# Kernel tuning notes

Measured on AMD Instinct MI355X. Metric: run time of the kernel, lower is better.

The kernel has to match this reference:

```python
import jax, jax.numpy as jnp
import numpy as np

B, H, S, D = 2, 16, 2048, 128


def alibi_slopes(n_heads: int) -> jnp.ndarray:
    # Standard ALiBi geometric slopes: 2^(-8*(h+1)/n_heads)
    h = jnp.arange(n_heads, dtype=jnp.float32)
    return jnp.exp2(-8.0 * (h + 1.0) / n_heads)


def setup_inputs() -> dict:
    key = jax.random.key(0)
    kq, kk, kv = jax.random.split(key, 3)
    q = jax.random.normal(kq, (B, H, S, D), dtype=jnp.float32)
    k = jax.random.normal(kk, (B, H, S, D), dtype=jnp.float32)
    v = jax.random.normal(kv, (B, H, S, D), dtype=jnp.float32)
    return {"q": q, "k": k, "v": v}


def reference(q, k, v):
    # FlexAttention forward: causal block mask + ALiBi score_mod, default scale 1/sqrt(D)
    d = q.shape[-1]
    scale = 1.0 / jnp.sqrt(jnp.asarray(d, dtype=q.dtype))
    slopes = alibi_slopes(q.shape[1]).astype(q.dtype)  # [H]

    scores = jnp.einsum("bhqd,bhkd->bhqk", q, k) * scale  # [B,H,S,S]
    q_idx = jnp.arange(q.shape[2])[:, None]   # [S,1]
    kv_idx = jnp.arange(k.shape[2])[None, :]  # [1,S]
    # score_mod: score + slopes[h] * (kv - q)  (bias <= 0 in causal region)
    bias = slopes[None, :, None, None] * (kv_idx - q_idx).astype(q.dtype)[None, None]
    scores = scores + bias
    causal = q_idx >= kv_idx  # [S,S]
    neg_inf = jnp.asarray(-jnp.inf, dtype=scores.dtype)
    scores = jnp.where(causal[None, None], scores, neg_inf)
    probs = jax.nn.softmax(scores, axis=-1)
    return jnp.einsum("bhqk,bhkd->bhqd", probs, v)
```

## Files before the change

### kernel.cpp

```cpp
#include <hip/hip_runtime.h>
#include <hip/hip_bf16.h>

#define BB 2
#define HH 16
#define SS 2048
#define DD 128

constexpr int BM = 64;
constexpr int BN = 64;
constexpr int NW = 4;
constexpr size_t SD = (size_t)SS * DD;
constexpr size_t KV_ELEMS = (size_t)BB * HH * SS * DD;

typedef __bf16 bf16_t;
typedef unsigned int u32;
typedef __attribute__((ext_vector_type(8))) __bf16 bf16x8;
typedef __attribute__((ext_vector_type(4))) __bf16 bf16x4;
typedef __attribute__((ext_vector_type(4))) float floatx4;
typedef __attribute__((ext_vector_type(16))) float floatx16;
typedef __attribute__((ext_vector_type(4))) unsigned int u32x4;

__device__ __forceinline__ void dma16(const void* g, void* l) {
    __builtin_amdgcn_global_load_lds(
        (const __attribute__((address_space(1))) unsigned int*)g,
        (__attribute__((address_space(3))) unsigned int*)l,
        16, 0, 0);
}

__device__ __forceinline__ u32 cvt_pk_bf16(float lo, float hi) {
    u32 r;
    asm("v_cvt_pk_bf16_f32 %0, %1, %2" : "=v"(r) : "v"(lo), "v"(hi));
    return r;
}

__device__ __forceinline__ void plane32_swap(u32& a, u32& b) {
    asm("v_permlane32_swap_b32 %0, %1" : "+v"(a), "+v"(b));
}

__global__ __launch_bounds__(256)
void prep_kv(const float* __restrict__ kp, const float* __restrict__ vp,
             bf16_t* __restrict__ kbf, bf16_t* __restrict__ vtbf)
{
    __shared__ __align__(16) bf16_t VT[64][140];

    const int tid  = threadIdx.x;
    const int kv0  = blockIdx.x * BN;
    const size_t bh = blockIdx.y;

    const float* kb = kp + bh * SD;
    const float* vb = vp + bh * SD;
    bf16_t* ko = kbf  + bh * SD;
    bf16_t* vo = vtbf + bh * (size_t)DD * SS;

    #pragma unroll
    for (int i = 0; i < 8; ++i) {
        int idx4 = tid + i * 256;
        int row  = idx4 >> 5;
        int c4   = idx4 & 31;
        float4 val = *reinterpret_cast<const float4*>(vb + (size_t)(kv0 + row) * DD + c4 * 4);
        bf16x4 o;
        o[0] = (bf16_t)val.x; o[1] = (bf16_t)val.y; o[2] = (bf16_t)val.z; o[3] = (bf16_t)val.w;
        *reinterpret_cast<bf16x4*>(&VT[row][c4 * 4]) = o;
    }

    #pragma unroll
    for (int i = 0; i < 8; ++i) {
        int idx4 = tid + i * 256;
        int row  = idx4 >> 5;
        int c4   = idx4 & 31;
        float4 val = *reinterpret_cast<const float4*>(kb + (size_t)(kv0 + row) * DD + c4 * 4);
        bf16x4 o;
        o[0] = (bf16_t)val.x; o[1] = (bf16_t)val.y; o[2] = (bf16_t)val.z; o[3] = (bf16_t)val.w;
        *reinterpret_cast<bf16x4*>(ko + (size_t)(kv0 + row) * DD + c4 * 4) = o;
    }

    __syncthreads();

    const int kv8 = (tid & 7) * 8;
    const int dg  = tid >> 3;
    #pragma unroll
    for (int i = 0; i < 4; ++i) {
        int d = dg + i * 32;
        bf16x8 w;
        #pragma unroll
        for (int j = 0; j < 8; ++j)
            w[j] = VT[kv8 + j][d];
        *reinterpret_cast<bf16x8*>(vo + (size_t)d * SS + kv0 + kv8) = w;
    }
}

__global__ __launch_bounds__(256, 2)
void flexattn_fwd_bf16(const float* __restrict__ qp, const bf16_t* __restrict__ kbf,
                       const bf16_t* __restrict__ vtbf, float* __restrict__ op)
{
    __shared__ __align__(16) bf16_t KV[2][2][8192];

    const int tid   = threadIdx.x;
    const int wave  = tid >> 6;
    const int lane  = tid & 63;
    const int l31   = lane & 31;
    const int lhalf = lane >> 5;
    const int qh    = wave >> 1;
    const int kh    = wave & 1;

    const int lid  = blockIdx.y * gridDim.x + blockIdx.x;
    const int xcd  = lid & 7;
    const int slot = lid >> 3;
    const int nl   = xcd * ((SS / BM) * BB * HH / 8) + slot;
    const int bh   = nl >> 5;
    const int qt   = 31 - (nl & 31);
    const int h    = bh & (HH - 1);
    const int q0   = qt * BM;

    const float LOG2E  = 1.4426950408889634f;
    const float sscale = 0.08838834764831845f * LOG2E;
    const float slope  = __builtin_amdgcn_exp2f(-8.0f * (float)(h + 1) / (float)HH);
    const float bscale = slope * LOG2E;

    const float*  qb = qp   + (size_t)bh * SD;
    const bf16_t* kb = kbf  + (size_t)bh * SD;
    const bf16_t* vt = vtbf + (size_t)bh * (size_t)DD * SS;
    float*        ob = op   + (size_t)bh * SD;

    const int q = q0 + qh * 32 + l31;

    int koff[4], voff[4];
    #pragma unroll
    for (int i = 0; i < 4; ++i) {
        int c   = wave * 256 + i * 64 + lane;
        int kv  = c >> 4;
        int col = (c & 15) ^ (kv & 15);
        koff[i] = kv * 256 + col * 16;
        int d  = c >> 3;
        int jp = c & 7;
        int j  = jp ^ (d & 7) ^ (((d >> 3) & 1) << 2);
        voff[i] = (d * SS + j * 8) * 2;
    }

    auto dma_tile = [&](int kt, int b) {
        const char* kg = (const char*)kb + (size_t)kt * (BN * DD * 2);
        const char* vg = (const char*)vt + (size_t)kt * (BN * 2);
        char* kl = (char*)&KV[b][0][0];
        char* vl = (char*)&KV[b][1][0];
        #pragma unroll
        for (int i = 0; i < 4; ++i) {
            int base = (wave * 256 + i * 64) * 16;
            dma16(kg + koff[i], kl + base);
            dma16(vg + voff[i], vl + base);
        }
    };

    bf16x8 qf[8];
    #pragma unroll
    for (int dc = 0; dc < 8; ++dc) {
        const float* qs = qb + (size_t)q * DD + dc * 16 + lhalf * 8;
        float4 a = *reinterpret_cast<const float4*>(qs);
        float4 b = *reinterpret_cast<const float4*>(qs + 4);
        qf[dc][0] = (bf16_t)a.x; qf[dc][1] = (bf16_t)a.y;
        qf[dc][2] = (bf16_t)a.z; qf[dc][3] = (bf16_t)a.w;
        qf[dc][4] = (bf16_t)b.x; qf[dc][5] = (bf16_t)b.y;
        qf[dc][6] = (bf16_t)b.z; qf[dc][7] = (bf16_t)b.w;
    }

    dma_tile(0, 0);

    floatx16 zero16;
    #pragma unroll
    for (int i = 0; i < 16; ++i) zero16[i] = 0.f;

    floatx16 o[4];
    #pragma unroll
    for (int t = 0; t < 4; ++t) o[t] = zero16;
    float l_i = 0.f;

    const int kbase0 = kh * 32 - q;

    int kfo[8];
    const int krow = kh * 32 + l31;
    #pragma unroll
    for (int dc = 0; dc < 8; ++dc)
        kfo[dc] = krow * 256 + (((dc * 2 + lhalf) ^ (krow & 15)) * 16);

    int vfo[4][2];
    #pragma unroll
    for (int t = 0; t < 4; ++t) {
        int row = t * 32 + l31;
        int key = (row & 7) ^ (((row >> 3) & 1) << 2);
        #pragma unroll
        for (int m = 0; m < 2; ++m)
            vfo[t][m] = row * 128 + (((kh * 4 + m * 2 + lhalf) ^ key) * 16);
    }

    __syncthreads();

    for (int kt = 0; kt <= qt; ++kt) {
        const int kv0 = kt * BN;
        const int b   = kt & 1;
        if (kt < qt) dma_tile(kt + 1, b ^ 1);

        const char* kl = (const char*)&KV[b][0][0];
        const char* vl = (const char*)&KV[b][1][0];
        const bool diag = (kt == qt);

        if (!(diag && qh == 0 && kh == 1)) {
            floatx16 acc = zero16;
            __builtin_amdgcn_s_setprio(1);
            #pragma unroll
            for (int dc = 0; dc < 8; ++dc) {
                bf16x8 kf = *reinterpret_cast<const bf16x8*>(kl + kfo[dc]);
                acc = __builtin_amdgcn_mfma_f32_32x32x16_bf16(kf, qf[dc], acc, 0, 0, 0);
            }
            __builtin_amdgcn_s_setprio(0);

            float pv[16];
            float rs = 0.f;
            #pragma unroll
            for (int reg = 0; reg < 16; ++reg) {
                int row   = (reg & 3) + 8 * (reg >> 2) + 4 * lhalf;
                int delta = kv0 + kbase0 + row;
                float sval = acc[reg] * sscale + (bscale * (float)delta - 8.0f);
                if (diag && delta > 0) sval = -3.0e38f;
                float p = __builtin_amdgcn_exp2f(sval);
                pv[reg] = p;
                rs += p;
            }
            l_i += rs;

            u32 pk[8];
            #pragma unroll
            for (int i = 0; i < 8; ++i)
                pk[i] = cvt_pk_bf16(pv[2 * i], pv[2 * i + 1]);
            plane32_swap(pk[0], pk[2]);
            plane32_swap(pk[1], pk[3]);
            plane32_swap(pk[4], pk[6]);
            plane32_swap(pk[5], pk[7]);
            u32x4 pw0 = {pk[0], pk[1], pk[2], pk[3]};
            u32x4 pw1 = {pk[4], pk[5], pk[6], pk[7]};
            bf16x8 pfrag0 = __builtin_bit_cast(bf16x8, pw0);
            bf16x8 pfrag1 = __builtin_bit_cast(bf16x8, pw1);

            __builtin_amdgcn_s_setprio(1);
            #pragma unroll
            for (int t = 0; t < 4; ++t) {
                bf16x8 vf0 = *reinterpret_cast<const bf16x8*>(vl + vfo[t][0]);
                o[t] = __builtin_amdgcn_mfma_f32_32x32x16_bf16(vf0, pfrag0, o[t], 0, 0, 0);
                bf16x8 vf1 = *reinterpret_cast<const bf16x8*>(vl + vfo[t][1]);
                o[t] = __builtin_amdgcn_mfma_f32_32x32x16_bf16(vf1, pfrag1, o[t], 0, 0, 0);
            }
            __builtin_amdgcn_s_setprio(0);
        }

        __syncthreads();
    }

    float lq = l_i + __shfl_xor(l_i, 32);

    float* OX = reinterpret_cast<float*>(&KV[0][0][0]);
    float* LX = reinterpret_cast<float*>(&KV[1][0][0]);

    if (kh == 1) {
        #pragma unroll
        for (int t = 0; t < 4; ++t) {
            #pragma unroll
            for (int reg = 0; reg < 16; ++reg) {
                int d = t * 32 + (reg & 3) + 8 * (reg >> 2) + 4 * lhalf;
                OX[d * 64 + qh * 32 + l31] = o[t][reg];
            }
        }
        if (lane < 32) LX[qh * 32 + l31] = lq;
    }
    __syncthreads();
    if (kh == 0) {
        const float linv = 1.0f / (lq + LX[qh * 32 + l31]);
        #pragma unroll
        for (int t = 0; t < 4; ++t) {
            #pragma unroll
            for (int r4 = 0; r4 < 4; ++r4) {
                int dbase = t * 32 + 8 * r4 + 4 * lhalf;
                float4 w;
                w.x = (o[t][r4 * 4 + 0] + OX[(dbase + 0) * 64 + qh * 32 + l31]) * linv;
                w.y = (o[t][r4 * 4 + 1] + OX[(dbase + 1) * 64 + qh * 32 + l31]) * linv;
                w.z = (o[t][r4 * 4 + 2] + OX[(dbase + 2) * 64 + qh * 32 + l31]) * linv;
                w.w = (o[t][r4 * 4 + 3] + OX[(dbase + 3) * 64 + qh * 32 + l31]) * linv;
                *reinterpret_cast<float4*>(ob + (size_t)q * DD + dbase) = w;
            }
        }
    }
}

extern "C" void kernel_launch(void* const* d_in, const int* in_sizes, int n_in,
                              void* d_out, int out_size, void* d_ws, size_t ws_size,
                              hipStream_t stream) {
    const float* q = (const float*)d_in[0];
    const float* k = (const float*)d_in[1];
    const float* v = (const float*)d_in[2];
    float* out = (float*)d_out;

    bf16_t* kbf  = (bf16_t*)d_ws;
    bf16_t* vtbf = kbf + KV_ELEMS;
    prep_kv<<<dim3(SS / BN, BB * HH), 256, 0, stream>>>(k, v, kbf, vtbf);
    flexattn_fwd_bf16<<<dim3(SS / BM, BB * HH), 256, 0, stream>>>(q, kbf, vtbf, out);
}
```

Measured before the change: 187.2 us.

## Pre-swizzle V into MFMA fragment order and load it directly from global

The V-transpose prep kernel now writes V in the exact per-lane MFMA fragment order, so the attention kernel loads V fragments straight from global/L2 into registers instead of staging them through LDS. This halves LDS usage (K only double-buffered), which lets launch bounds rise from 2 to 3 blocks per CU for more occupancy. The trade-off is that V now comes from global memory on every tile, with loads issued early to hide latency, and the extra occupancy raises register pressure.

```diff
diff --git a/kernel.cpp b/kernel.cpp
--- a/kernel.cpp
+++ b/kernel.cpp
@@ -76,24 +76,28 @@
 
     __syncthreads();
 
-    const int kv8 = (tid & 7) * 8;
-    const int dg  = tid >> 3;
+    const int kv8   = (tid & 7) * 8;
+    const int dg    = tid >> 3;
+    const int kh    = kv8 >> 5;
+    const int m     = (kv8 >> 4) & 1;
+    const int lhalf = (kv8 >> 3) & 1;
     #pragma unroll
     for (int i = 0; i < 4; ++i) {
-        int d = dg + i * 32;
         bf16x8 w;
         #pragma unroll
         for (int j = 0; j < 8; ++j)
-            w[j] = VT[kv8 + j][d];
-        *reinterpret_cast<bf16x8*>(vo + (size_t)d * SS + kv0 + kv8) = w;
-    }
-}
-
-__global__ __launch_bounds__(256, 2)
+            w[j] = VT[kv8 + j][i * 32 + dg];
+        size_t chunk = (size_t)(((blockIdx.x * 2 + kh) * 4 + i) * 2 + m);
+        *reinterpret_cast<bf16x8*>(vo + chunk * 512 + lhalf * 256 + dg * 8) = w;
+    }
+}
+
+__global__ __launch_bounds__(256, 3)
 void flexattn_fwd_bf16(const float* __restrict__ qp, const bf16_t* __restrict__ kbf,
                        const bf16_t* __restrict__ vtbf, float* __restrict__ op)
 {
-    __shared__ __align__(16) bf16_t KV[2][2][8192];
+    __shared__ __align__(16) bf16_t Kbuf[2][8192];
+    __shared__ float LX[64];
 
     const int tid   = threadIdx.x;
     const int wave  = tid >> 6;
@@ -124,29 +128,22 @@
 
     const int q = q0 + qh * 32 + l31;
 
-    int koff[4], voff[4];
+    int koff[4];
     #pragma unroll
     for (int i = 0; i < 4; ++i) {
         int c   = wave * 256 + i * 64 + lane;
         int kv  = c >> 4;
         int col = (c & 15) ^ (kv & 15);
         koff[i] = kv * 256 + col * 16;
-        int d  = c >> 3;
-        int jp = c & 7;
-        int j  = jp ^ (d & 7) ^ (((d >> 3) & 1) << 2);
-        voff[i] = (d * SS + j * 8) * 2;
     }
 
     auto dma_tile = [&](int kt, int b) {
         const char* kg = (const char*)kb + (size_t)kt * (BN * DD * 2);
-        const char* vg = (const char*)vt + (size_t)kt * (BN * 2);
-        char* kl = (char*)&KV[b][0][0];
-        char* vl = (char*)&KV[b][1][0];
+        char* kl = (char*)&Kbuf[b][0];
         #pragma unroll
         for (int i = 0; i < 4; ++i) {
             int base = (wave * 256 + i * 64) * 16;
             dma16(kg + koff[i], kl + base);
-            dma16(vg + voff[i], vl + base);
         }
     };
 
@@ -181,25 +178,23 @@
     for (int dc = 0; dc < 8; ++dc)
         kfo[dc] = krow * 256 + (((dc * 2 + lhalf) ^ (krow & 15)) * 16);
 
-    int vfo[4][2];
-    #pragma unroll
-    for (int t = 0; t < 4; ++t) {
-        int row = t * 32 + l31;
-        int key = (row & 7) ^ (((row >> 3) & 1) << 2);
-        #pragma unroll
-        for (int m = 0; m < 2; ++m)
-            vfo[t][m] = row * 128 + (((kh * 4 + m * 2 + lhalf) ^ key) * 16);
-    }
+    const bf16_t* vfb = vt + (size_t)lane * 8;
 
     __syncthreads();
 
     for (int kt = 0; kt <= qt; ++kt) {
         const int kv0 = kt * BN;
         const int b   = kt & 1;
+
+        const bf16_t* vsrc = vfb + (size_t)((kt * 2 + kh) * 8) * 512;
+        bf16x8 vfA0 = *reinterpret_cast<const bf16x8*>(vsrc);
+        bf16x8 vfA1 = *reinterpret_cast<const bf16x8*>(vsrc + 512);
+        bf16x8 vfA2 = *reinterpret_cast<const bf16x8*>(vsrc + 1024);
+        bf16x8 vfA3 = *reinterpret_cast<const bf16x8*>(vsrc + 1536);
+
         if (kt < qt) dma_tile(kt + 1, b ^ 1);
 
-        const char* kl = (const char*)&KV[b][0][0];
-        const char* vl = (const char*)&KV[b][1][0];
+        const char* kl = (const char*)&Kbuf[b][0];
         const bool diag = (kt == qt);
 
         if (!(diag && qh == 0 && kh == 1)) {
@@ -211,6 +206,11 @@
                 acc = __builtin_amdgcn_mfma_f32_32x32x16_bf16(kf, qf[dc], acc, 0, 0, 0);
             }
             __builtin_amdgcn_s_setprio(0);
+
+            bf16x8 vfB0 = *reinterpret_cast<const bf16x8*>(vsrc + 2048);
+            bf16x8 vfB1 = *reinterpret_cast<const bf16x8*>(vsrc + 2560);
+            bf16x8 vfB2 = *reinterpret_cast<const bf16x8*>(vsrc + 3072);
+            bf16x8 vfB3 = *reinterpret_cast<const bf16x8*>(vsrc + 3584);
 
             float pv[16];
             float rs = 0.f;
@@ -240,13 +240,14 @@
             bf16x8 pfrag1 = __builtin_bit_cast(bf16x8, pw1);
 
             __builtin_amdgcn_s_setprio(1);
-            #pragma unroll
-            for (int t = 0; t < 4; ++t) {
-                bf16x8 vf0 = *reinterpret_cast<const bf16x8*>(vl + vfo[t][0]);
-                o[t] = __builtin_amdgcn_mfma_f32_32x32x16_bf16(vf0, pfrag0, o[t], 0, 0, 0);
-                bf16x8 vf1 = *reinterpret_cast<const bf16x8*>(vl + vfo[t][1]);
-                o[t] = __builtin_amdgcn_mfma_f32_32x32x16_bf16(vf1, pfrag1, o[t], 0, 0, 0);
-            }
+            o[0] = __builtin_amdgcn_mfma_f32_32x32x16_bf16(vfA0, pfrag0, o[0], 0, 0, 0);
+            o[0] = __builtin_amdgcn_mfma_f32_32x32x16_bf16(vfA1, pfrag1, o[0], 0, 0, 0);
+            o[1] = __builtin_amdgcn_mfma_f32_32x32x16_bf16(vfA2, pfrag0, o[1], 0, 0, 0);
+            o[1] = __builtin_amdgcn_mfma_f32_32x32x16_bf16(vfA3, pfrag1, o[1], 0, 0, 0);
+            o[2] = __builtin_amdgcn_mfma_f32_32x32x16_bf16(vfB0, pfrag0, o[2], 0, 0, 0);
+            o[2] = __builtin_amdgcn_mfma_f32_32x32x16_bf16(vfB1, pfrag1, o[2], 0, 0, 0);
+            o[3] = __builtin_amdgcn_mfma_f32_32x32x16_bf16(vfB2, pfrag0, o[3], 0, 0, 0);
+            o[3] = __builtin_amdgcn_mfma_f32_32x32x16_bf16(vfB3, pfrag1, o[3], 0, 0, 0);
             __builtin_amdgcn_s_setprio(0);
         }
 
@@ -255,8 +256,7 @@
 
     float lq = l_i + __shfl_xor(l_i, 32);
 
-    float* OX = reinterpret_cast<float*>(&KV[0][0][0]);
-    float* LX = reinterpret_cast<float*>(&KV[1][0][0]);
+    float* OX = reinterpret_cast<float*>(&Kbuf[0][0]);
 
     if (kh == 1) {
         #pragma unroll
```

New measurement: 204.0 us. 9.0% more time.
